# Kernel optimization log

Measured on AMD Instinct MI355X. Metric: run time of the kernel, lower is better.

Reference implementation:

```python
import jax, jax.numpy as jnp
from jax import lax
import numpy as np

N, I, O = 64, 8, 8
B = 512
S_EX, S_PHI, S_RHO = 10, 60, 60  # S_phi must equal S_rho (alpha loops feed S_rho-sized h into the GRUs)
N_ACTIONS, N_ROLES = 5, 7


def _gru(x, h, Wih, Whh, bih, bhh):
    # torch.nn.GRUCell math
    gi = x @ Wih.T + bih
    gh = h @ Whh.T + bhh
    ir, iz, inn = jnp.split(gi, 3, axis=-1)
    hr, hz, hn = jnp.split(gh, 3, axis=-1)
    r = jax.nn.sigmoid(ir + hr)
    zg = jax.nn.sigmoid(iz + hz)
    n = jnp.tanh(inn + r * hn)
    return (1.0 - zg) * n + zg * h


def setup_inputs() -> dict:
    key = jax.random.key(0)
    ks = jax.random.split(key, 24)
    f32 = jnp.float32
    z = jax.random.normal(ks[0], (B, N, S_EX), f32)
    dz = jax.random.normal(ks[1], (B, N, S_EX), f32)
    has = (jax.random.uniform(ks[2], (B, N)) < 0.9).astype(f32)
    adj = (jnp.triu(jax.random.uniform(ks[3], (N, N)), 1) > 0.7).astype(jnp.int32)

    def lin(k, o, i):
        return (jax.random.normal(k, (o, i), f32) * np.float32(1.0 / np.sqrt(i)))

    d = dict(z=z, dz=dz, has=has, adj=adj)
    d['Wih_f'] = lin(ks[4], 3 * S_PHI, S_RHO)
    d['Whh_f'] = lin(ks[5], 3 * S_PHI, S_PHI)
    d['bih_f'] = jax.random.normal(ks[6], (3 * S_PHI,), f32) * 0.02
    d['bhh_f'] = jax.random.normal(ks[7], (3 * S_PHI,), f32) * 0.02
    d['Wih_b'] = lin(ks[8], 3 * S_PHI, S_RHO)
    d['Whh_b'] = lin(ks[9], 3 * S_PHI, S_PHI)
    d['bih_b'] = jax.random.normal(ks[10], (3 * S_PHI,), f32) * 0.02
    d['bhh_b'] = jax.random.normal(ks[11], (3 * S_PHI,), f32) * 0.02
    d['Wf'] = lin(ks[12], S_RHO, S_PHI + 2 * S_EX)
    d['bf'] = jax.random.normal(ks[13], (S_RHO,), f32) * 0.02
    d['Wb'] = lin(ks[14], S_RHO, S_PHI + 2 * S_EX)
    d['bb'] = jax.random.normal(ks[15], (S_RHO,), f32) * 0.02
    d['Wa'] = lin(ks[16], N_ACTIONS, 2 * S_PHI)
    d['ba'] = jax.random.normal(ks[17], (N_ACTIONS,), f32) * 0.02
    d['Wc'] = lin(ks[18], 1, 2 * S_PHI)
    d['bc'] = jax.random.normal(ks[19], (1,), f32) * 0.02
    d['Wu'] = lin(ks[20], N_ROLES, 2 * S_RHO)
    d['bu'] = jax.random.normal(ks[21], (N_ROLES,), f32) * 0.02
    return d


def reference(z, dz, has, adj,
              Wih_f, Whh_f, bih_f, bhh_f,
              Wih_b, Whh_b, bih_b, bhh_b,
              Wf, bf, Wb, bb, Wa, ba, Wc, bc, Wu, bu):
    Bn, Nn = has.shape
    dt = z.dtype
    adjf = adj.astype(dt)

    # ---- forward sweep over nodes in ascending order ----
    def fwd_outer(rho, i):
        def inner(h, j):
            hn = _gru(rho[j], h, Wih_f, Whh_f, bih_f, bhh_f)
            blend = adjf[j, i] * has[:, j][:, None]  # edge exists AND source node present
            return h + blend * (hn - h), None
        h, _ = lax.scan(inner, jnp.zeros((Bn, S_PHI), dt), jnp.arange(Nn))
        rho_i = jnp.tanh(jnp.concatenate([h, z[:, i], dz[:, i]], 1) @ Wf.T + bf)
        return rho.at[i].set(rho_i), None

    rho_f, _ = lax.scan(fwd_outer, jnp.zeros((Nn, Bn, S_RHO), dt), jnp.arange(Nn))

    # ---- backward sweep over nodes in descending order ----
    def bwd_outer(rho, i):
        def inner(h, j):
            hn = _gru(rho[j], h, Wih_b, Whh_b, bih_b, bhh_b)
            blend = adjf[i, j] * has[:, j][:, None]  # out-edges of i, visited descending
            return h + blend * (hn - h), None
        h, _ = lax.scan(inner, jnp.zeros((Bn, S_PHI), dt), jnp.arange(Nn - 1, -1, -1))
        rho_i = jnp.concatenate([h, z[:, i], dz[:, i]], 1) @ Wb.T + bb
        return rho.at[i].set(rho_i), None

    rho_b, _ = lax.scan(bwd_outer, jnp.zeros((Nn, Bn, S_RHO), dt), jnp.arange(Nn - 1, -1, -1))

    # ---- aggregate outputs (last O nodes) and inputs (first I nodes) ----
    h = jnp.zeros((Bn, S_RHO), dt)
    for i in range(N - O, N):
        hn = _gru(rho_f[i], h, Wih_f, Whh_f, bih_f, bhh_f)
        h = h + has[:, i][:, None] * (hn - h)
    alpha_f = h
    h = jnp.zeros((Bn, S_RHO), dt)
    for i in reversed(range(I)):
        hn = _gru(rho_b[i], h, Wih_b, Whh_b, bih_b, bhh_b)
        h = h + has[:, i][:, None] * (hn - h)
    alpha_b = h

    ab = jnp.concatenate([alpha_f, alpha_b], 1)
    omega = ab @ Wa.T + ba          # [B, 5]
    value = ab @ Wc.T + bc          # [B, 1]

    feats = jnp.concatenate([rho_f, rho_b], -1)           # [N, B, 2*S_rho]
    psi = jnp.einsum('nbs,rs->brn', feats, Wu) + bu[None, :, None]  # [B, 7, N]
    m = has[:, None, :]
    psi = -60.0 * (1.0 - m) + psi * m  # interpolate(-60, psi, has)

    instr_prob = jax.nn.softmax(omega, axis=1)
    role_prob = jax.nn.softmax(psi, axis=2)
    return instr_prob, role_prob, value
```

## Files before the change

kernel.cpp:

```cpp
#include <hip/hip_runtime.h>
#include <hip/hip_bf16.h>

#define NN 64
#define BATCH 512
#define SP 60
#define SG 180
#define SEX 10
#define CATD 80
#define NA 5
#define NR 7
#define OO 8
#define II 8

typedef unsigned long long u64;
typedef unsigned short u16;
typedef unsigned int u32;
typedef unsigned char u8;

#define OFF_Z     0
#define OFF_DZ    327680
#define OFF_HAS   655360
#define OFF_WIHF  688128
#define OFF_WHHF  698928
#define OFF_BIHF  709728
#define OFF_BHHF  709908
#define OFF_WIHB  710088
#define OFF_WHHB  720888
#define OFF_BIHB  731688
#define OFF_BHHB  731868
#define OFF_WF    732048
#define OFF_BF    736848
#define OFF_WB    736908
#define OFF_BB    741708
#define OFF_WA    741768
#define OFF_BA    742368
#define OFF_WC    742373
#define OFF_BC    742493
#define OFF_WU    742494
#define OFF_BU    743334
#define CONV_TOTAL 743341
#define OFF_FLAG  743342
#define OFF_RHOF  743344
#define OFF_RHOB  (OFF_RHOF + 1966080)
#define OFF_ALF   (OFF_RHOB + 1966080)
#define OFF_ALB   (OFF_ALF + 30720)
#define OUT_TOTAL 232448

typedef _Float16 f16;
typedef _Float16 half2_t __attribute__((ext_vector_type(2)));
typedef _Float16 f16x8 __attribute__((ext_vector_type(8)));
typedef float f32x4 __attribute__((ext_vector_type(4)));

__device__ __forceinline__ float us2f(u16 v){
  return __uint_as_float(((u32)v) << 16);
}
__device__ __forceinline__ u16 f2bf(float f){
  __hip_bfloat16 h = __float2bfloat16(f);
  return *reinterpret_cast<u16*>(&h);
}
__device__ __forceinline__ float rcp_(float x){ return __builtin_amdgcn_rcpf(x); }
__device__ __forceinline__ float sigm(float x){
  return rcp_(1.f + __expf(-x));
}
__device__ __forceinline__ float tanh_(float x){
  float e = __expf(2.f*fabsf(x));
  float t = 1.f - 2.f*rcp_(e + 1.f);
  return copysignf(t, x);
}
__device__ __forceinline__ u32 pack2(float a, float b){
  half2_t h; h[0] = (f16)a; h[1] = (f16)b;
  return __builtin_bit_cast(u32, h);
}
__device__ __forceinline__ float fdot2_(u32 a, u32 b, float c){
  return __builtin_amdgcn_fdot2(__builtin_bit_cast(half2_t, a),
                                __builtin_bit_cast(half2_t, b), c, false);
}
__device__ __forceinline__ f16x8 bc16(uint4 v){ return __builtin_bit_cast(f16x8, v); }
__device__ __forceinline__ f32x4 mfma16(f16x8 a, f16x8 b, f32x4 c){
  return __builtin_amdgcn_mfma_f32_16x16x32_f16(a, b, c, 0, 0, 0);
}

__global__ __launch_bounds__(256) void conv_in(
  const void* z, const void* dz, const void* has,
  const void* WihF, const void* WhhF, const void* bihF, const void* bhhF,
  const void* WihB, const void* WhhB, const void* bihB, const void* bhhB,
  const void* Wf_, const void* bf_, const void* Wb_, const void* bb_,
  const void* Wa, const void* ba, const void* Wc, const void* bc,
  const void* Wu, const void* bu, float* ws)
{
  __shared__ int sIsBf;
  const int tid = threadIdx.x;
  if (tid < 64){
    const u32* w = (const u32*)has;
    int f = 0;
    #pragma unroll
    for (int k=0;k<4;k++) f |= (w[tid*4 + k] == 0x3F803F80u) ? 1 : 0;
    u64 m = __ballot(f != 0);
    if (tid == 0) sIsBf = (m != 0ULL) ? 1 : 0;
  }
  __syncthreads();
  const int isbf = sIsBf;
  if (blockIdx.x == 0 && tid == 0) ws[OFF_FLAG] = (float)isbf;
  int idx = blockIdx.x*256 + tid;
  if (idx >= CONV_TOTAL) return;
  const void* src; int loc;
  if      (idx < OFF_DZ  ){ src=z;    loc=idx-OFF_Z;    }
  else if (idx < OFF_HAS ){ src=dz;   loc=idx-OFF_DZ;   }
  else if (idx < OFF_WIHF){ src=has;  loc=idx-OFF_HAS;  }
  else if (idx < OFF_WHHF){ src=WihF; loc=idx-OFF_WIHF; }
  else if (idx < OFF_BIHF){ src=WhhF; loc=idx-OFF_WHHF; }
  else if (idx < OFF_BHHF){ src=bihF; loc=idx-OFF_BIHF; }
  else if (idx < OFF_WIHB){ src=bhhF; loc=idx-OFF_BHHF; }
  else if (idx < OFF_WHHB){ src=WihB; loc=idx-OFF_WIHB; }
  else if (idx < OFF_BIHB){ src=WhhB; loc=idx-OFF_WHHB; }
  else if (idx < OFF_BHHB){ src=bihB; loc=idx-OFF_BIHB; }
  else if (idx < OFF_WF  ){ src=bhhB; loc=idx-OFF_BHHB; }
  else if (idx < OFF_BF  ){ src=Wf_;  loc=idx-OFF_WF;   }
  else if (idx < OFF_WB  ){ src=bf_;  loc=idx-OFF_BF;   }
  else if (idx < OFF_BB  ){ src=Wb_;  loc=idx-OFF_WB;   }
  else if (idx < OFF_WA  ){ src=bb_;  loc=idx-OFF_BB;   }
  else if (idx < OFF_BA  ){ src=Wa;   loc=idx-OFF_WA;   }
  else if (idx < OFF_WC  ){ src=ba;   loc=idx-OFF_BA;   }
  else if (idx < OFF_BC  ){ src=Wc;   loc=idx-OFF_WC;   }
  else if (idx < OFF_WU  ){ src=bc;   loc=idx-OFF_BC;   }
  else if (idx < OFF_BU  ){ src=Wu;   loc=idx-OFF_WU;   }
  else                    { src=bu;   loc=idx-OFF_BU;   }
  float v = isbf ? us2f(((const u16*)src)[loc]) : ((const float*)src)[loc];
  ws[idx] = v;
}

__global__ __launch_bounds__(256, 2) void dir_kernel(const int* __restrict__ adj,
                                                     float* __restrict__ ws)
{
  const int tid = threadIdx.x;
  const int w   = tid >> 6;
  const int u   = tid & 63;
  const int ml  = u & 15;
  const int q   = u >> 4;
  const int bid = blockIdx.x;
  const int bwd = bid >> 8;
  const int bp  = (bid & 255) << 1;

  const float* Wih  = ws + (bwd ? OFF_WIHB : OFF_WIHF);
  const float* Whh  = ws + (bwd ? OFF_WHHB : OFF_WHHF);
  const float* bih  = ws + (bwd ? OFF_BIHB : OFF_BIHF);
  const float* bhh  = ws + (bwd ? OFF_BHHB : OFF_BHHF);
  const float* Wcat = ws + (bwd ? OFF_WB   : OFF_WF);
  const float* bcat = ws + (bwd ? OFF_BB   : OFF_BF);
  const float* zc   = ws + OFF_Z;
  const float* dzc  = ws + OFF_DZ;
  const float* hasc = ws + OFF_HAS;
  float* rho   = ws + (bwd ? OFF_RHOB : OFF_RHOF);
  float* alpha = ws + (bwd ? OFF_ALB  : OFF_ALF);

  __shared__ uint4 sH4[2][65][9];
  __shared__ uint4 sRhoPad[2][8];
  __shared__ uint4 sRhoHist[2][8][8];
  __shared__ float sZdc[2][NN][SP];
  __shared__ u32 sZp[2][NN][5];
  __shared__ u32 sDZp[2][NN][5];
  __shared__ float sHas[2][NN];
  __shared__ u64 sRowM[NN];
  __shared__ u8 sConsL[NN][64];
  __shared__ int sConsCnt[NN];

  #define ROWB(E,I) ((char*)&sH4[(E)][(I)][0])
  const u32 BIASW = 0x3C000000u;

  {
    if (tid < 64){
      u64 rowm = 0;
      for (int j=0;j<64;j++) rowm |= ((u64)(adj[tid*64+j]!=0))<<j;
      sRowM[tid] = rowm;
    }
    if (tid < 128){
      const int e = tid >> 6, n = tid & 63;
      sHas[e][n] = hasc[(bp+e)*NN + n];
    }
    for (int idx=tid; idx<2*65*9; idx+=256){
      uint4 v = {0,0,0,0};
      if ((idx % 9) == 7) v.w = BIASW;
      ((uint4*)sH4)[idx] = v;
    }
    if (tid < 16){ uint4 v={0,0,0,0}; if ((tid&7)==7) v.w = BIASW; ((uint4*)sRhoPad)[tid]=v; }
    if (tid < 128){ uint4 v={0,0,0,0}; if ((tid&7)==7) v.w = BIASW; ((uint4*)sRhoHist)[tid]=v; }
    for (int idx=tid; idx<2*NN*5; idx+=256){
      int e = idx/(NN*5), rem = idx%(NN*5), n2=rem/5, p2=rem%5;
      sZp [e][n2][p2] = pack2(zc [(size_t)(bp+e)*NN*SEX + n2*SEX + 2*p2],
                              zc [(size_t)(bp+e)*NN*SEX + n2*SEX + 2*p2+1]);
      sDZp[e][n2][p2] = pack2(dzc[(size_t)(bp+e)*NN*SEX + n2*SEX + 2*p2],
                              dzc[(size_t)(bp+e)*NN*SEX + n2*SEX + 2*p2+1]);
    }
  }
  __syncthreads();
  if (tid < 64){
    u64 cm = 0;
    if (bwd) for (int i2=0;i2<64;i2++) cm |= ((sRowM[i2]>>tid)&1ULL)<<i2;
    u64 m = bwd ? cm : sRowM[tid];
    int c = 0;
    while (m){ int i2 = (int)__builtin_ctzll(m); m &= m-1; sConsL[tid][c++] = (u8)i2; }
    sConsCnt[tid] = c;
  }
  {
    const int uu = tid & 63;
    const int tw = tid >> 6;
    if (uu < SP){
      u32 wz[10];
      #pragma unroll
      for (int p=0;p<10;p++)
        wz[p] = pack2(Wcat[uu*CATD + 60 + 2*p], Wcat[uu*CATD + 60 + 2*p + 1]);
      const float bb0 = bcat[uu];
      for (int et=tw; et<2*NN; et+=4){
        const int e = et >> 6, t2 = et & 63;
        float c = bb0;
        #pragma unroll
        for (int p=0;p<5;p++){
          c = fdot2_(wz[p],   sZp [e][t2][p], c);
          c = fdot2_(wz[5+p], sDZp[e][t2][p], c);
        }
        sZdc[e][t2][uu] = c;
      }
    }
  }

  f16x8 Ar[4], Az[4], Anh[2], Ani[2], Ac[2];
  {
    const int R = 16*w + ml;
    const bool rok = (R < SP);
    #pragma unroll
    for (int kt=0; kt<4; kt++){
      f16x8 vr, vz;
      #pragma unroll
      for (int j=0;j<8;j++){
        const int K = 32*kt + 8*q + j;
        float wr=0.f, wz2=0.f;
        if (rok){
          if (K < SP){ wr = Whh[R*SP+K]; wz2 = Whh[(60+R)*SP+K]; }
          else if (K >= 64 && K < 64+SP){ wr = Wih[R*SP+(K-64)]; wz2 = Wih[(60+R)*SP+(K-64)]; }
          else if (K == 127){ wr = bhh[R]+bih[R]; wz2 = bhh[60+R]+bih[60+R]; }
        }
        vr[j]=(f16)wr; vz[j]=(f16)wz2;
      }
      Ar[kt]=vr; Az[kt]=vz;
    }
    #pragma unroll
    for (int kt=0; kt<2; kt++){
      f16x8 vn, vi, vc;
      #pragma unroll
      for (int j=0;j<8;j++){
        const int K = 32*kt + 8*q + j;
        float wn=0.f, wi=0.f, wcv=0.f;
        if (rok){
          if (K < SP){ wn = Whh[(120+R)*SP+K]; wi = Wih[(120+R)*SP+K]; wcv = Wcat[R*CATD+K]; }
          else if (K == 63){ wn = bhh[120+R]; wi = bih[120+R]; }
        }
        vn[j]=(f16)wn; vi[j]=(f16)wi; vc[j]=(f16)wcv;
      }
      Anh[kt]=vn; Ani[kt]=vi; Ac[kt]=vc;
    }
  }
  __syncthreads();

  auto gates = [&](f32x4 Dr, f32x4 Dz, f32x4 Dn, f32x4 Gn,
                   char* rowb, bool wr, float bl){
    char* rp = rowb + 32*w + 8*q;
    uint2 h2 = *(uint2*)rp;
    half2_t ha = __builtin_bit_cast(half2_t, h2.x);
    half2_t hb = __builtin_bit_cast(half2_t, h2.y);
    float hold[4] = { (float)ha[0], (float)ha[1], (float)hb[0], (float)hb[1] };
    float hw[4];
    #pragma unroll
    for (int reg=0;reg<4;reg++){
      float r_ = sigm(Dr[reg]);
      float zg = sigm(Dz[reg]);
      float nv = tanh_(Gn[reg] + r_*Dn[reg]);
      float hn_ = (1.f - zg)*nv + zg*hold[reg];
      hw[reg] = (bl != 0.f) ? hn_ : hold[reg];
    }
    if (wr && !(w==3 && q==3)){
      uint2 o; o.x = pack2(hw[0],hw[1]); o.y = pack2(hw[2],hw[3]);
      *(uint2*)rp = o;
    }
  };

  auto fullpass = [&](f16x8 Bh0, f16x8 Bh1, f16x8 Br0, f16x8 Br1,
                      f32x4 Gn, char* rowb, bool wr, float bl){
    f32x4 Dr={0,0,0,0}, Dz={0,0,0,0}, Dn={0,0,0,0};
    Dr = mfma16(Ar[0], Bh0, Dr); Dr = mfma16(Ar[1], Bh1, Dr);
    Dr = mfma16(Ar[2], Br0, Dr); Dr = mfma16(Ar[3], Br1, Dr);
    Dz = mfma16(Az[0], Bh0, Dz); Dz = mfma16(Az[1], Bh1, Dz);
    Dz = mfma16(Az[2], Br0, Dz); Dz = mfma16(Az[3], Br1, Dz);
    Dn = mfma16(Anh[0], Bh0, Dn); Dn = mfma16(Anh[1], Bh1, Dn);
    gates(Dr, Dz, Dn, Gn, rowb, wr, bl);
  };

  int t = bwd ? 63 : 0;
  const int dt = bwd ? -1 : 1;
  for (int s=0; s<64; s++, t+=dt){
    const int cnt = sConsCnt[t];
    const float bl0 = sHas[0][t];
    const float bl1 = sHas[1][t];
    const bool act = (cnt > 0) && (bl0 != 0.f || bl1 != 0.f);
    const bool g1  = act && (cnt > 16);

    int ci0 = 64, ci1 = 64;
    f16x8 Bh0e0={}, Bh1e0={}, Bh0e1={}, Bh1e1={};
    f16x8 Ch0e0={}, Ch1e0={}, Ch0e1={}, Ch1e1={};
    if (act){
      ci0 = (ml < cnt) ? (int)sConsL[t][ml] : 64;
      Bh0e0 = bc16(sH4[0][ci0][q]); Bh1e0 = bc16(sH4[0][ci0][4+q]);
      Bh0e1 = bc16(sH4[1][ci0][q]); Bh1e1 = bc16(sH4[1][ci0][4+q]);
      if (g1){
        ci1 = (16 + ml < cnt) ? (int)sConsL[t][16 + ml] : 64;
        Ch0e0 = bc16(sH4[0][ci1][q]); Ch1e0 = bc16(sH4[0][ci1][4+q]);
        Ch0e1 = bc16(sH4[1][ci1][q]); Ch1e1 = bc16(sH4[1][ci1][4+q]);
      }
    }

    {
      const f16x8 H00 = bc16(sH4[0][t][q]);
      const f16x8 H01 = bc16(sH4[0][t][4+q]);
      const f16x8 H10 = bc16(sH4[1][t][q]);
      const f16x8 H11 = bc16(sH4[1][t][4+q]);
      f32x4 Rv0 = {0,0,0,0}, Rv1 = {0,0,0,0};
      Rv0 = mfma16(Ac[0], H00, Rv0);
      Rv1 = mfma16(Ac[0], H10, Rv1);
      Rv0 = mfma16(Ac[1], H01, Rv0);
      Rv1 = mfma16(Ac[1], H11, Rv1);
      const int row = 16*w + 4*q + ml;
      if (ml < 4 && row < SP){
        float v0 = Rv0[0], v1 = Rv1[0];
        v0 = (ml==1) ? Rv0[1] : v0;  v1 = (ml==1) ? Rv1[1] : v1;
        v0 = (ml==2) ? Rv0[2] : v0;  v1 = (ml==2) ? Rv1[2] : v1;
        v0 = (ml==3) ? Rv0[3] : v0;  v1 = (ml==3) ? Rv1[3] : v1;
        v0 += sZdc[0][t][row];
        v1 += sZdc[1][t][row];
        if (!bwd){ v0 = tanh_(v0); v1 = tanh_(v1); }
        *(f16*)((char*)&sRhoPad[0][0] + 2*row) = (f16)v0;
        *(f16*)((char*)&sRhoPad[1][0] + 2*row) = (f16)v1;
        const int slot = bwd ? t : (t - (NN-OO));
        if (slot >= 0 && slot < 8){
          *(f16*)((char*)&sRhoHist[0][slot][0] + 2*row) = (f16)v0;
          *(f16*)((char*)&sRhoHist[1][slot][0] + 2*row) = (f16)v1;
        }
        rho[((size_t)t*BATCH + bp  )*SP + row] = v0;
        rho[((size_t)t*BATCH + bp+1)*SP + row] = v1;
      }
    }
    __syncthreads();

    if (act){
      const f16x8 Br0e0 = bc16(sRhoPad[0][q]);
      const f16x8 Br1e0 = bc16(sRhoPad[0][4+q]);
      const f16x8 Br0e1 = bc16(sRhoPad[1][q]);
      const f16x8 Br1e1 = bc16(sRhoPad[1][4+q]);
      f32x4 Gn0={0,0,0,0}, Gn1={0,0,0,0};
      Gn0 = mfma16(Ani[0], Br0e0, Gn0);  Gn1 = mfma16(Ani[0], Br0e1, Gn1);
      Gn0 = mfma16(Ani[1], Br1e0, Gn0);  Gn1 = mfma16(Ani[1], Br1e1, Gn1);
      f32x4 Pr0={0,0,0,0}, Pr1={0,0,0,0};
      Pr0 = mfma16(Ar[2], Br0e0, Pr0);   Pr1 = mfma16(Ar[2], Br0e1, Pr1);
      Pr0 = mfma16(Ar[3], Br1e0, Pr0);   Pr1 = mfma16(Ar[3], Br1e1, Pr1);
      f32x4 Pz0={0,0,0,0}, Pz1={0,0,0,0};
      Pz0 = mfma16(Az[2], Br0e0, Pz0);   Pz1 = mfma16(Az[2], Br0e1, Pz1);
      Pz0 = mfma16(Az[3], Br1e0, Pz0);   Pz1 = mfma16(Az[3], Br1e1, Pz1);

      {
        f32x4 Dr0=Pr0, Dz0=Pz0, Dn0={0,0,0,0};
        f32x4 Dr1=Pr1, Dz1=Pz1, Dn1={0,0,0,0};
        Dr0 = mfma16(Ar[0], Bh0e0, Dr0);  Dr1 = mfma16(Ar[0], Bh0e1, Dr1);
        Dr0 = mfma16(Ar[1], Bh1e0, Dr0);  Dr1 = mfma16(Ar[1], Bh1e1, Dr1);
        Dz0 = mfma16(Az[0], Bh0e0, Dz0);  Dz1 = mfma16(Az[0], Bh0e1, Dz1);
        Dz0 = mfma16(Az[1], Bh1e0, Dz0);  Dz1 = mfma16(Az[1], Bh1e1, Dz1);
        Dn0 = mfma16(Anh[0], Bh0e0, Dn0); Dn1 = mfma16(Anh[0], Bh0e1, Dn1);
        Dn0 = mfma16(Anh[1], Bh1e0, Dn0); Dn1 = mfma16(Anh[1], Bh1e1, Dn1);
        gates(Dr0, Dz0, Dn0, Gn0, ROWB(0,ci0), ml < cnt, bl0);
        gates(Dr1, Dz1, Dn1, Gn1, ROWB(1,ci0), ml < cnt, bl1);
      }
      if (g1){
        f32x4 Dr0=Pr0, Dz0=Pz0, Dn0={0,0,0,0};
        f32x4 Dr1=Pr1, Dz1=Pz1, Dn1={0,0,0,0};
        Dr0 = mfma16(Ar[0], Ch0e0, Dr0);  Dr1 = mfma16(Ar[0], Ch0e1, Dr1);
        Dr0 = mfma16(Ar[1], Ch1e0, Dr0);  Dr1 = mfma16(Ar[1], Ch1e1, Dr1);
        Dz0 = mfma16(Az[0], Ch0e0, Dz0);  Dz1 = mfma16(Az[0], Ch0e1, Dz1);
        Dz0 = mfma16(Az[1], Ch1e0, Dz0);  Dz1 = mfma16(Az[1], Ch1e1, Dz1);
        Dn0 = mfma16(Anh[0], Ch0e0, Dn0); Dn1 = mfma16(Anh[0], Ch0e1, Dn1);
        Dn0 = mfma16(Anh[1], Ch1e0, Dn0); Dn1 = mfma16(Anh[1], Ch1e1, Dn1);
        gates(Dr0, Dz0, Dn0, Gn0, ROWB(0,ci1), 16 + ml < cnt, bl0);
        gates(Dr1, Dz1, Dn1, Gn1, ROWB(1,ci1), 16 + ml < cnt, bl1);
      }
      for (int p=2; 16*p < cnt; p++){
        const int idxp = 16*p + ml;
        const int ci = (idxp < cnt) ? (int)sConsL[t][idxp] : 64;
        fullpass(bc16(sH4[0][ci][q]), bc16(sH4[0][ci][4+q]),
                 Br0e0, Br1e0, Gn0, ROWB(0,ci), idxp < cnt, bl0);
        fullpass(bc16(sH4[1][ci][q]), bc16(sH4[1][ci][4+q]),
                 Br0e1, Br1e1, Gn1, ROWB(1,ci), idxp < cnt, bl1);
      }
    }
    __syncthreads();
  }

  for (int s2=0; s2<8; s2++){
    const int i = bwd ? (7 - s2) : (NN - OO + s2);
    const int slot = bwd ? i : (i - (NN-OO));
    const f16x8 Th00 = bc16(sH4[0][64][q]);
    const f16x8 Th01 = bc16(sH4[0][64][4+q]);
    const f16x8 Th10 = bc16(sH4[1][64][q]);
    const f16x8 Th11 = bc16(sH4[1][64][4+q]);
    const f16x8 Tr00 = bc16(sRhoHist[0][slot][q]);
    const f16x8 Tr01 = bc16(sRhoHist[0][slot][4+q]);
    const f16x8 Tr10 = bc16(sRhoHist[1][slot][q]);
    const f16x8 Tr11 = bc16(sRhoHist[1][slot][4+q]);
    f32x4 Gt0={0,0,0,0}, Gt1={0,0,0,0};
    Gt0 = mfma16(Ani[0], Tr00, Gt0);  Gt1 = mfma16(Ani[0], Tr10, Gt1);
    Gt0 = mfma16(Ani[1], Tr01, Gt0);  Gt1 = mfma16(Ani[1], Tr11, Gt1);
    __syncthreads();
    fullpass(Th00, Th01, Tr00, Tr01, Gt0, ROWB(0,64), ml==0, sHas[0][i]);
    fullpass(Th10, Th11, Tr10, Tr11, Gt1, ROWB(1,64), ml==0, sHas[1][i]);
    __syncthreads();
  }
  if (tid < SP){
    alpha[(size_t)(bp  )*SP + tid] = (float)*(const f16*)(ROWB(0,64) + 2*tid);
    alpha[(size_t)(bp+1)*SP + tid] = (float)*(const f16*)(ROWB(1,64) + 2*tid);
  }
  #undef ROWB
}

__global__ __launch_bounds__(256, 1) void head_kernel(float* __restrict__ ws,
                                                      void* __restrict__ outp)
{
  const int b = blockIdx.x;
  const int tid = threadIdx.x;
  const int isbf = (ws[OFF_FLAG] != 0.f);
  const float* hasc   = ws + OFF_HAS;
  const float* WaC    = ws + OFF_WA;
  const float* baC    = ws + OFF_BA;
  const float* WcC    = ws + OFF_WC;
  const float* bcC    = ws + OFF_BC;
  const float* WuC    = ws + OFF_WU;
  const float* buC    = ws + OFF_BU;
  const float* rhoF   = ws + OFF_RHOF;
  const float* rhoB   = ws + OFF_RHOB;
  const float* alphaF = ws + OFF_ALF;
  const float* alphaB = ws + OFF_ALB;

  __shared__ float sF[NN][122];
  __shared__ float sAB[120];
  __shared__ float sWu[NR*120];
  __shared__ float sHasR[NN];
  __shared__ float sPsi[NR][NN];
  __shared__ float sOm[NA];

  auto wout = [&](int idx, float v){
    if (isbf) ((u16*)outp)[idx] = f2bf(v);
    else      ((float*)outp)[idx] = v;
  };

  for (int idx=tid; idx<NN*SP; idx+=256){
    int n = idx/SP, s = idx%SP;
    sF[n][s]    = rhoF[((size_t)n*BATCH + b)*SP + s];
    sF[n][60+s] = rhoB[((size_t)n*BATCH + b)*SP + s];
  }
  for (int idx=tid; idx<120; idx+=256)
    sAB[idx] = (idx<60) ? alphaF[(size_t)b*SP + idx] : alphaB[(size_t)b*SP + idx-60];
  for (int idx=tid; idx<NR*120; idx+=256) sWu[idx] = WuC[idx];
  for (int idx=tid; idx<NN; idx+=256) sHasR[idx] = hasc[b*NN + idx];
  __syncthreads();

  for (int idx=tid; idx<NR*NN; idx+=256){
    int r = idx/NN, n = idx%NN;
    const float2* fn = (const float2*)&sF[n][0];
    const float2* wr = (const float2*)&sWu[r*120];
    float acc = buC[r];
    #pragma unroll 6
    for (int s2=0;s2<60;s2++){
      float2 a = fn[s2], c = wr[s2];
      acc += a.x*c.x;
      acc += a.y*c.y;
    }
    sPsi[r][n] = (sHasR[n] != 0.f) ? acc : -60.f;
  }
  if (tid >= 64 && tid < 64+NA){
    int a = tid - 64;
    float acc = baC[a];
    for (int s=0;s<120;s++) acc += sAB[s]*WaC[a*120+s];
    sOm[a] = acc;
  }
  if (tid == 70){
    float acc = bcC[0];
    for (int s=0;s<120;s++) acc += sAB[s]*WcC[s];
    wout(2560 + BATCH*NR*NN + b, acc);
  }
  __syncthreads();

  if (tid < NR*32){
    const int r = tid >> 5, l = tid & 31;
    float v0 = sPsi[r][l], v1 = sPsi[r][l+32];
    float m = fmaxf(v0, v1);
    #pragma unroll
    for (int o=16;o>0;o>>=1) m = fmaxf(m, __shfl_xor(m, o, 64));
    float e0 = __expf(v0 - m), e1 = __expf(v1 - m);
    float ssum = e0 + e1;
    #pragma unroll
    for (int o=16;o>0;o>>=1) ssum += __shfl_xor(ssum, o, 64);
    float rinv = 1.f/ssum;
    wout(2560 + (size_t)b*NR*NN + r*NN + l,    e0*rinv);
    wout(2560 + (size_t)b*NR*NN + r*NN + l+32, e1*rinv);
  }
  if (tid == 224){
    float m = -1e30f;
    for (int a=0;a<NA;a++) m = fmaxf(m, sOm[a]);
    float e[NA]; float ssum = 0.f;
    for (int a=0;a<NA;a++){ e[a] = __expf(sOm[a]-m); ssum += e[a]; }
    for (int a=0;a<NA;a++) wout(b*NA + a, e[a]/ssum);
  }
}

extern "C" void kernel_launch(void* const* d_in, const int* in_sizes, int n_in,
                              void* d_out, int out_size, void* d_ws, size_t ws_size,
                              hipStream_t stream)
{
  const int* adj = (const int*)d_in[3];
  float* ws = (float*)d_ws;

  conv_in<<<(CONV_TOTAL+255)/256, 256, 0, stream>>>(
      d_in[0], d_in[1], d_in[2],
      d_in[4], d_in[5], d_in[6], d_in[7],
      d_in[8], d_in[9], d_in[10], d_in[11],
      d_in[12], d_in[13], d_in[14], d_in[15],
      d_in[16], d_in[17], d_in[18], d_in[19],
      d_in[20], d_in[21], ws);

  dir_kernel<<<512, 256, 0, stream>>>(adj, ws);

  head_kernel<<<512, 256, 0, stream>>>(ws, d_out);
}
```

Measured before the change: 252.4 us.

## Pack both batch elements into one MFMA tile when consumer count is small

When a node has at most 8 consumers, the two batch elements are packed into the 16 MFMA columns: lanes 0-7 handle element 0 and lanes 8-15 handle element 1. A single set of gate MFMAs then replaces the separate per-element passes. The rho computation is packed the same way, with both elements sharing one MFMA pair. The aim is to roughly halve MFMA and LDS work on the common sparse-consumer steps. The cost is extra branching, and a second code path that must stay consistent with the general one.

```diff
diff --git a/kernel.cpp b/kernel.cpp
--- a/kernel.cpp
+++ b/kernel.cpp
@@ -300,13 +300,22 @@
     const int cnt = sConsCnt[t];
     const float bl0 = sHas[0][t];
     const float bl1 = sHas[1][t];
-    const bool act = (cnt > 0) && (bl0 != 0.f || bl1 != 0.f);
-    const bool g1  = act && (cnt > 16);
-
-    int ci0 = 64, ci1 = 64;
+    const bool act   = (cnt > 0) && (bl0 != 0.f || bl1 != 0.f);
+    const bool fastp = act && (cnt <= 8);
+    const bool slowp = act && (cnt > 8);
+    const bool g1    = act && (cnt > 16);
+
+    int ci0 = 64, ci1 = 64, cim = 64;
+    const int eh = ml >> 3;
+    f16x8 Bm0={}, Bm1={};
     f16x8 Bh0e0={}, Bh1e0={}, Bh0e1={}, Bh1e1={};
     f16x8 Ch0e0={}, Ch1e0={}, Ch0e1={}, Ch1e1={};
-    if (act){
+    if (fastp){
+      const int sl = ml & 7;
+      cim = (sl < cnt) ? (int)sConsL[t][sl] : 64;
+      Bm0 = bc16(sH4[eh][cim][q]);
+      Bm1 = bc16(sH4[eh][cim][4+q]);
+    } else if (slowp){
       ci0 = (ml < cnt) ? (int)sConsL[t][ml] : 64;
       Bh0e0 = bc16(sH4[0][ci0][q]); Bh1e0 = bc16(sH4[0][ci0][4+q]);
       Bh0e1 = bc16(sH4[1][ci0][q]); Bh1e1 = bc16(sH4[1][ci0][4+q]);
@@ -318,38 +327,43 @@
     }
 
     {
-      const f16x8 H00 = bc16(sH4[0][t][q]);
-      const f16x8 H01 = bc16(sH4[0][t][4+q]);
-      const f16x8 H10 = bc16(sH4[1][t][q]);
-      const f16x8 H11 = bc16(sH4[1][t][4+q]);
-      f32x4 Rv0 = {0,0,0,0}, Rv1 = {0,0,0,0};
-      Rv0 = mfma16(Ac[0], H00, Rv0);
-      Rv1 = mfma16(Ac[0], H10, Rv1);
-      Rv0 = mfma16(Ac[1], H01, Rv0);
-      Rv1 = mfma16(Ac[1], H11, Rv1);
-      const int row = 16*w + 4*q + ml;
-      if (ml < 4 && row < SP){
-        float v0 = Rv0[0], v1 = Rv1[0];
-        v0 = (ml==1) ? Rv0[1] : v0;  v1 = (ml==1) ? Rv1[1] : v1;
-        v0 = (ml==2) ? Rv0[2] : v0;  v1 = (ml==2) ? Rv1[2] : v1;
-        v0 = (ml==3) ? Rv0[3] : v0;  v1 = (ml==3) ? Rv1[3] : v1;
-        v0 += sZdc[0][t][row];
-        v1 += sZdc[1][t][row];
-        if (!bwd){ v0 = tanh_(v0); v1 = tanh_(v1); }
-        *(f16*)((char*)&sRhoPad[0][0] + 2*row) = (f16)v0;
-        *(f16*)((char*)&sRhoPad[1][0] + 2*row) = (f16)v1;
+      const int em = (ml >> 2) & 1;
+      const f16x8 Hm0 = bc16(sH4[em][t][q]);
+      const f16x8 Hm1 = bc16(sH4[em][t][4+q]);
+      f32x4 Rv = {0,0,0,0};
+      Rv = mfma16(Ac[0], Hm0, Rv);
+      Rv = mfma16(Ac[1], Hm1, Rv);
+      const int row = 16*w + 4*q + (ml & 3);
+      if (ml < 8 && row < SP){
+        const int m3 = ml & 3;
+        float vv = Rv[0];
+        vv = (m3==1) ? Rv[1] : vv;
+        vv = (m3==2) ? Rv[2] : vv;
+        vv = (m3==3) ? Rv[3] : vv;
+        vv += sZdc[em][t][row];
+        if (!bwd) vv = tanh_(vv);
+        *(f16*)((char*)&sRhoPad[em][0] + 2*row) = (f16)vv;
         const int slot = bwd ? t : (t - (NN-OO));
-        if (slot >= 0 && slot < 8){
-          *(f16*)((char*)&sRhoHist[0][slot][0] + 2*row) = (f16)v0;
-          *(f16*)((char*)&sRhoHist[1][slot][0] + 2*row) = (f16)v1;
-        }
-        rho[((size_t)t*BATCH + bp  )*SP + row] = v0;
-        rho[((size_t)t*BATCH + bp+1)*SP + row] = v1;
+        if (slot >= 0 && slot < 8)
+          *(f16*)((char*)&sRhoHist[em][slot][0] + 2*row) = (f16)vv;
+        rho[((size_t)t*BATCH + bp + em)*SP + row] = vv;
       }
     }
     __syncthreads();
 
-    if (act){
+    if (fastp){
+      const f16x8 Brm0 = bc16(sRhoPad[eh][q]);
+      const f16x8 Brm1 = bc16(sRhoPad[eh][4+q]);
+      f32x4 Gn={0,0,0,0};
+      Gn = mfma16(Ani[0], Brm0, Gn); Gn = mfma16(Ani[1], Brm1, Gn);
+      f32x4 Dr={0,0,0,0}, Dz={0,0,0,0}, Dn={0,0,0,0};
+      Dr = mfma16(Ar[2], Brm0, Dr); Dr = mfma16(Ar[3], Brm1, Dr);
+      Dr = mfma16(Ar[0], Bm0,  Dr); Dr = mfma16(Ar[1], Bm1,  Dr);
+      Dz = mfma16(Az[2], Brm0, Dz); Dz = mfma16(Az[3], Brm1, Dz);
+      Dz = mfma16(Az[0], Bm0,  Dz); Dz = mfma16(Az[1], Bm1,  Dz);
+      Dn = mfma16(Anh[0], Bm0, Dn); Dn = mfma16(Anh[1], Bm1, Dn);
+      gates(Dr, Dz, Dn, Gn, ROWB(eh, cim), (ml & 7) < cnt, eh ? bl1 : bl0);
+    } else if (slowp){
       const f16x8 Br0e0 = bc16(sRhoPad[0][q]);
       const f16x8 Br1e0 = bc16(sRhoPad[0][4+q]);
       const f16x8 Br0e1 = bc16(sRhoPad[1][q]);
```

Result: faster. 246.8 us (-2.2%).
